# Optimization experiments

Hardware: AMD Instinct MI355X
Metric: run time of the kernel (lower is better)

The kernel has to match this reference:

```python
import jax, jax.numpy as jnp
import numpy as np

N_NODES = 50000
N_EDGES = 600000
N_GRAPHS = 64


def _linear_init(key, fan_in, fan_out):
    # torch nn.Linear default: U(-1/sqrt(fan_in), 1/sqrt(fan_in))
    s = 1.0 / np.sqrt(fan_in)
    kw, kb = jax.random.split(key)
    W = jax.random.uniform(kw, (fan_in, fan_out), jnp.float32, -s, s)
    b = jax.random.uniform(kb, (fan_out,), jnp.float32, -s, s)
    return W, b


def setup_inputs() -> dict:
    key = jax.random.key(0)
    ks = jax.random.split(key, 7)
    x = jax.random.normal(ks[0], (N_NODES, 128), jnp.float32)
    edge_index = jax.random.randint(ks[1], (2, N_EDGES), 0, N_NODES, dtype=jnp.int32).astype(jnp.int64)
    batch = jnp.sort(jax.random.randint(ks[2], (N_NODES,), 0, N_GRAPHS, dtype=jnp.int32)).astype(jnp.int64)
    W1, b1 = _linear_init(ks[3], 128, 256)
    W2, b2 = _linear_init(ks[4], 256, 256)
    W3, b3 = _linear_init(ks[5], 256, 128)
    W4, b4 = _linear_init(ks[6], 128, 10)
    return dict(x=x, edge_index=edge_index, batch=batch,
                W1=W1, b1=b1, W2=W2, b2=b2, W3=W3, b3=b3, W4=W4, b4=b4)


def _gcn_conv(h, src, dst, W, b, n_nodes):
    # PyG GCNConv: add self-loops (src/dst already include them),
    # symmetric normalization D^{-1/2} (A+I) D^{-1/2} h W + b.
    h = h @ W                                      # [N, Cout]
    deg = jax.ops.segment_sum(jnp.ones(src.shape[0], h.dtype), dst, num_segments=n_nodes)
    dinv = jnp.where(deg > 0, jax.lax.rsqrt(deg), 0.0)
    norm = dinv[src] * dinv[dst]                   # [E+N]
    msg = h[src] * norm[:, None]                   # gather + scale per edge
    agg = jax.ops.segment_sum(msg, dst, num_segments=n_nodes)  # scatter-add
    return agg + b


def reference(x, edge_index, batch, W1, b1, W2, b2, W3, b3, W4, b4):
    n = x.shape[0]
    loops = jnp.arange(n, dtype=edge_index.dtype)
    src = jnp.concatenate([edge_index[0], loops])
    dst = jnp.concatenate([edge_index[1], loops])
    # GCNBlock (activate_last=True since dense layers follow)
    h = jax.nn.relu(_gcn_conv(x, src, dst, W1, b1, n))
    h = jax.nn.relu(_gcn_conv(h, src, dst, W2, b2, n))
    # global_mean_pool over batch segments
    sums = jax.ops.segment_sum(h, batch, num_segments=N_GRAPHS)          # [G, 256]
    counts = jax.ops.segment_sum(jnp.ones((n,), h.dtype), batch, num_segments=N_GRAPHS)
    g = sums / jnp.maximum(counts, 1.0)[:, None]
    # DenseBlock [256 -> 128 -> 10], activate_last=False
    g = jax.nn.relu(g @ W3 + b3)
    return g @ W4 + b4
```

## Files before the change

kernel.cpp:

```cpp
#include <hip/hip_runtime.h>

typedef unsigned short u16;
typedef unsigned int u32;
typedef __attribute__((ext_vector_type(8))) short s16x8;
typedef __attribute__((ext_vector_type(4))) float f32x4;

#define NN 50000
#define NE 600000
#define NG 64

__device__ __forceinline__ u16 f2bf(float f) {
    u32 u = __float_as_uint(f);
    u32 r = (u + 0x7fffu + ((u >> 16) & 1u)) >> 16;
    return (u16)r;
}
__device__ __forceinline__ float bf2f(u16 h) {
    return __uint_as_float(((u32)h) << 16);
}
__device__ __forceinline__ void gll16(const void* g, void* l) {
    __builtin_amdgcn_global_load_lds((const __attribute__((address_space(1))) u32*)g,
                                     (__attribute__((address_space(3))) u32*)l, 16, 0, 0);
}

__global__ void k_hist(const int* __restrict__ dst, int* __restrict__ cnt, int ne) {
    int e = blockIdx.x * blockDim.x + threadIdx.x;
    if (e < ne) atomicAdd(&cnt[dst[e]], 1);
}

__global__ __launch_bounds__(256)
void k_scan1(const int* __restrict__ cnt, int* __restrict__ bsum, int n) {
    int i = blockIdx.x * 256 + threadIdx.x;
    int v = (i < n) ? cnt[i] : 0;
#pragma unroll
    for (int off = 32; off > 0; off >>= 1) v += __shfl_down(v, off, 64);
    __shared__ int ws[4];
    int lane = threadIdx.x & 63, w = threadIdx.x >> 6;
    if (lane == 0) ws[w] = v;
    __syncthreads();
    if (threadIdx.x == 0) bsum[blockIdx.x] = ws[0] + ws[1] + ws[2] + ws[3];
}

__global__ __launch_bounds__(256)
void k_scan2(int* __restrict__ bsum, int nb) {
    int t = threadIdx.x;
    int v = (t < nb) ? bsum[t] : 0;
    int lane = t & 63, w = t >> 6;
    int inc = v;
#pragma unroll
    for (int off = 1; off < 64; off <<= 1) {
        int x = __shfl_up(inc, off, 64);
        if (lane >= off) inc += x;
    }
    __shared__ int wtot[4];
    if (lane == 63) wtot[w] = inc;
    __syncthreads();
    int wo = 0;
    for (int j = 0; j < w; ++j) wo += wtot[j];
    if (t < nb) bsum[t] = wo + inc - v;
}

__global__ __launch_bounds__(256)
void k_scan3(const int* __restrict__ cnt, const int* __restrict__ boff,
             int* __restrict__ rowptr, int* __restrict__ cursor,
             float* __restrict__ dinv, int n) {
    int i = blockIdx.x * 256 + threadIdx.x;
    int v = (i < n) ? cnt[i] : 0;
    int lane = threadIdx.x & 63, w = threadIdx.x >> 6;
    int inc = v;
#pragma unroll
    for (int off = 1; off < 64; off <<= 1) {
        int x = __shfl_up(inc, off, 64);
        if (lane >= off) inc += x;
    }
    __shared__ int wtot[4];
    if (lane == 63) wtot[w] = inc;
    __syncthreads();
    int wo = boff[blockIdx.x];
    for (int j = 0; j < w; ++j) wo += wtot[j];
    if (i < n) {
        int excl = wo + inc - v;
        rowptr[i] = excl;
        cursor[i] = excl;
        dinv[i] = rsqrtf(1.0f + (float)v);
        if (i == n - 1) rowptr[n] = excl + v;
    }
}

__global__ void k_fill(const int* __restrict__ src, const int* __restrict__ dst,
                       int* __restrict__ cursor, int* __restrict__ csr_src, int ne) {
    int e = blockIdx.x * blockDim.x + threadIdx.x;
    if (e < ne) {
        int pos = atomicAdd(&cursor[dst[e]], 1);
        csr_src[pos] = src[e];
    }
}

__device__ __forceinline__ void wsplit_one(const float* W, u16* Whi, u16* Wlo, int K, int N, int idx) {
    int n = idx / K, k = idx - n * K;
    float w = W[(size_t)k * N + n];
    u16 hi = f2bf(w);
    u16 lo = f2bf(w - bf2f(hi));
    Whi[idx] = hi;
    Wlo[idx] = lo;
}

__global__ __launch_bounds__(256)
void k_preamble(const float* __restrict__ x, u16* __restrict__ xbf,
                const float* __restrict__ W1, u16* __restrict__ w1hi, u16* __restrict__ w1lo,
                const float* __restrict__ W2, u16* __restrict__ w2hi, u16* __restrict__ w2lo,
                float* __restrict__ sums, int* __restrict__ cnt,
                const int* __restrict__ batch, float* __restrict__ counts) {
    const int XB = (NN * 32 + 255) / 256;
    const int CB = (NN + 255) / 256;
    int b = blockIdx.x, t = threadIdx.x;
    if (b < XB) {
        int i = b * 256 + t;
        if (i < NN * 32) {
            float4 v = ((const float4*)x)[i];
            ushort4 o;
            o.x = f2bf(v.x); o.y = f2bf(v.y); o.z = f2bf(v.z); o.w = f2bf(v.w);
            ((ushort4*)xbf)[i] = o;
        }
        return;
    }
    b -= XB;
    if (b < 128) { wsplit_one(W1, w1hi, w1lo, 128, 256, b * 256 + t); return; }
    b -= 128;
    if (b < 256) { wsplit_one(W2, w2hi, w2lo, 256, 256, b * 256 + t); return; }
    b -= 256;
    if (b < 64) { sums[b * 256 + t] = 0.f; return; }
    b -= 64;
    if (b < CB) {
        int i = b * 256 + t;
        if (i < NN) cnt[i] = 0;
        return;
    }
    b -= CB;
    if (b == 0) {
        __shared__ int lb[65];
        if (t <= 64) {
            int lo = 0, hi = NN;
            while (lo < hi) {
                int mid = (lo + hi) >> 1;
                if (batch[mid] < t) lo = mid + 1; else hi = mid;
            }
            lb[t] = lo;
        }
        __syncthreads();
        if (t < 64) counts[t] = (float)(lb[t + 1] - lb[t]);
    }
}

template<int C>
__global__ __launch_bounds__(256)
void k_agg_gather(const int* __restrict__ rowptr, const int* __restrict__ csr_src,
                  const float* __restrict__ dinv, const u16* __restrict__ hb,
                  u16* __restrict__ out, int n) {
    constexpr int V = C / 64;
    int node = (blockIdx.x * blockDim.x + threadIdx.x) >> 6;
    int lane = threadIdx.x & 63;
    if (node >= n) return;
    int beg = rowptr[node], end = rowptr[node + 1];
    int m = end - beg;
    float di = dinv[node];
    float a0[V], a1[V];
    if constexpr (V == 4) {
        uint2 v = ((const uint2*)hb)[(size_t)node * 64 + lane];
        a0[0] = bf2f((u16)v.x) * di; a0[1] = bf2f((u16)(v.x >> 16)) * di;
        a0[2] = bf2f((u16)v.y) * di; a0[3] = bf2f((u16)(v.y >> 16)) * di;
        a1[0] = a1[1] = a1[2] = a1[3] = 0.f;
    } else {
        u32 v = ((const u32*)hb)[(size_t)node * 64 + lane];
        a0[0] = bf2f((u16)v) * di; a0[1] = bf2f((u16)(v >> 16)) * di;
        a1[0] = a1[1] = 0.f;
    }
    for (int base = 0; base < m; base += 64) {
        int c = m - base; if (c > 64) c = 64;
        int sid = 0; float w = 0.f;
        if (lane < c) { sid = csr_src[beg + base + lane]; w = dinv[sid]; }
        int e = 0;
        for (; e + 4 <= c; e += 4) {
            int   s0 = __shfl(sid, e, 64),   s1 = __shfl(sid, e + 1, 64);
            int   s2 = __shfl(sid, e + 2, 64), s3 = __shfl(sid, e + 3, 64);
            float w0 = __shfl(w, e, 64),     w1 = __shfl(w, e + 1, 64);
            float w2 = __shfl(w, e + 2, 64), w3 = __shfl(w, e + 3, 64);
            if constexpr (V == 4) {
                uint2 v0 = ((const uint2*)hb)[(size_t)s0 * 64 + lane];
                uint2 v1 = ((const uint2*)hb)[(size_t)s1 * 64 + lane];
                uint2 v2 = ((const uint2*)hb)[(size_t)s2 * 64 + lane];
                uint2 v3 = ((const uint2*)hb)[(size_t)s3 * 64 + lane];
                a0[0] += bf2f((u16)v0.x) * w0 + bf2f((u16)v2.x) * w2;
                a0[1] += bf2f((u16)(v0.x >> 16)) * w0 + bf2f((u16)(v2.x >> 16)) * w2;
                a0[2] += bf2f((u16)v0.y) * w0 + bf2f((u16)v2.y) * w2;
                a0[3] += bf2f((u16)(v0.y >> 16)) * w0 + bf2f((u16)(v2.y >> 16)) * w2;
                a1[0] += bf2f((u16)v1.x) * w1 + bf2f((u16)v3.x) * w3;
                a1[1] += bf2f((u16)(v1.x >> 16)) * w1 + bf2f((u16)(v3.x >> 16)) * w3;
                a1[2] += bf2f((u16)v1.y) * w1 + bf2f((u16)v3.y) * w3;
                a1[3] += bf2f((u16)(v1.y >> 16)) * w1 + bf2f((u16)(v3.y >> 16)) * w3;
            } else {
                u32 v0 = ((const u32*)hb)[(size_t)s0 * 64 + lane];
                u32 v1 = ((const u32*)hb)[(size_t)s1 * 64 + lane];
                u32 v2 = ((const u32*)hb)[(size_t)s2 * 64 + lane];
                u32 v3 = ((const u32*)hb)[(size_t)s3 * 64 + lane];
                a0[0] += bf2f((u16)v0) * w0 + bf2f((u16)v2) * w2;
                a0[1] += bf2f((u16)(v0 >> 16)) * w0 + bf2f((u16)(v2 >> 16)) * w2;
                a1[0] += bf2f((u16)v1) * w1 + bf2f((u16)v3) * w3;
                a1[1] += bf2f((u16)(v1 >> 16)) * w1 + bf2f((u16)(v3 >> 16)) * w3;
            }
        }
        for (; e < c; ++e) {
            int s0 = __shfl(sid, e, 64);
            float w0 = __shfl(w, e, 64);
            if constexpr (V == 4) {
                uint2 v0 = ((const uint2*)hb)[(size_t)s0 * 64 + lane];
                a0[0] += bf2f((u16)v0.x) * w0; a0[1] += bf2f((u16)(v0.x >> 16)) * w0;
                a0[2] += bf2f((u16)v0.y) * w0; a0[3] += bf2f((u16)(v0.y >> 16)) * w0;
            } else {
                u32 v0 = ((const u32*)hb)[(size_t)s0 * 64 + lane];
                a0[0] += bf2f((u16)v0) * w0; a0[1] += bf2f((u16)(v0 >> 16)) * w0;
            }
        }
    }
    if constexpr (V == 4) {
        uint2 o;
        o.x = (u32)f2bf((a0[0] + a1[0]) * di) | ((u32)f2bf((a0[1] + a1[1]) * di) << 16);
        o.y = (u32)f2bf((a0[2] + a1[2]) * di) | ((u32)f2bf((a0[3] + a1[3]) * di) << 16);
        ((uint2*)out)[(size_t)node * 64 + lane] = o;
    } else {
        ((u32*)out)[(size_t)node * 64 + lane] =
            (u32)f2bf((a0[0] + a1[0]) * di) | ((u32)f2bf((a0[1] + a1[1]) * di) << 16);
    }
}

__device__ __forceinline__ void stage_tile(u16* ldsbuf, const u16* A, const u16* Bhi,
                                           const u16* Blo, int bm, int k0, int M, int K,
                                           int wid, int lane) {
#pragma unroll
    for (int i = 0; i < 5; ++i) {
        int c = wid + 8 * i;
        const u16* gp;
        u32 lbase;
        if (c < 8) {
            int s = c * 64 + lane;
            int kga = s >> 7, row = s & 127;
            int rg = bm + row; if (rg >= M) rg = M - 1;
            gp = A + (size_t)rg * K + k0 + kga * 8;
            lbase = c * 512;
        } else if (c < 24) {
            int cc = c - 8;
            int s = cc * 64 + lane;
            int kgb = s >> 8, col = s & 255;
            gp = Bhi + (size_t)col * K + k0 + kgb * 8;
            lbase = 4096 + cc * 512;
        } else {
            int cc = c - 24;
            int s = cc * 64 + lane;
            int kgb = s >> 8, col = s & 255;
            gp = Blo + (size_t)col * K + k0 + kgb * 8;
            lbase = 12288 + cc * 512;
        }
        gll16(gp, ldsbuf + lbase);
    }
}

template<bool POOL>
__global__ __launch_bounds__(512)
void k_gemm_mfma(const u16* __restrict__ A, const u16* __restrict__ Bhi,
                 const u16* __restrict__ Blo,
                 const float* __restrict__ bias, u16* __restrict__ out_bf,
                 const int* __restrict__ batch, float* __restrict__ pool,
                 int M, int K) {
    __shared__ u16 lds[2][20480];
    const int tid = threadIdx.x, lane = tid & 63, wid = tid >> 6;
    const int bm = blockIdx.x * 128;
    const int wr = (wid >> 2) * 64, wc = (wid & 3) * 64;
    const int lr = lane & 15, kg = lane >> 4;

    f32x4 acc[4][4];
#pragma unroll
    for (int i = 0; i < 4; ++i)
#pragma unroll
        for (int j = 0; j < 4; ++j) acc[i][j] = (f32x4){0.f, 0.f, 0.f, 0.f};

    const int nt = K >> 5;
    stage_tile(lds[0], A, Bhi, Blo, bm, 0, M, K, wid, lane);
    __syncthreads();

    for (int t = 0; t < nt; ++t) {
        int cur = t & 1;
        if (t + 1 < nt)
            stage_tile(lds[cur ^ 1], A, Bhi, Blo, bm, (t + 1) << 5, M, K, wid, lane);
        const u16* lb = lds[cur];
        s16x8 a[4];
#pragma unroll
        for (int fm = 0; fm < 4; ++fm)
            a[fm] = *(const s16x8*)&lb[(u32)(kg * 128 + wr + fm * 16 + lr) * 8];
#pragma unroll
        for (int fn = 0; fn < 4; ++fn) {
            int col = wc + fn * 16 + lr;
            u32 sb = (u32)(kg * 256 + col) * 8;
            s16x8 bhi = *(const s16x8*)&lb[4096 + sb];
            s16x8 blo = *(const s16x8*)&lb[12288 + sb];
#pragma unroll
            for (int fm = 0; fm < 4; ++fm) {
                acc[fm][fn] = __builtin_amdgcn_mfma_f32_16x16x32_bf16(a[fm], bhi, acc[fm][fn], 0, 0, 0);
                acc[fm][fn] = __builtin_amdgcn_mfma_f32_16x16x32_bf16(a[fm], blo, acc[fm][fn], 0, 0, 0);
            }
        }
        __syncthreads();
    }

#pragma unroll
    for (int fn = 0; fn < 4; ++fn) {
        int col = wc + fn * 16 + lr;
        float bv = bias[col];
        if (!POOL) {
#pragma unroll
            for (int fm = 0; fm < 4; ++fm) {
                int rbase = bm + wr + fm * 16 + kg * 4;
#pragma unroll
                for (int r = 0; r < 4; ++r) {
                    int row = rbase + r;
                    if (row < M)
                        out_bf[(size_t)row * 256 + col] = f2bf(fmaxf(acc[fm][fn][r] + bv, 0.f));
                }
            }
        } else {
            int gcur = -1;
            float run = 0.f;
#pragma unroll
            for (int fm = 0; fm < 4; ++fm) {
                int rbase = bm + wr + fm * 16 + kg * 4;
#pragma unroll
                for (int r = 0; r < 4; ++r) {
                    int row = rbase + r;
                    if (row < M) {
                        int g = batch[row];
                        float v = fmaxf(acc[fm][fn][r] + bv, 0.f);
                        if (g != gcur) {
                            if (gcur >= 0) atomicAdd(&pool[gcur * 256 + col], run);
                            gcur = g;
                            run = 0.f;
                        }
                        run += v;
                    }
                }
            }
            if (gcur >= 0) atomicAdd(&pool[gcur * 256 + col], run);
        }
    }
}

__global__ __launch_bounds__(128)
void k_dense(const float* __restrict__ sums, const float* __restrict__ counts,
             const float* __restrict__ W3, const float* __restrict__ b3,
             const float* __restrict__ W4, const float* __restrict__ b4,
             float* __restrict__ out) {
    __shared__ float g[256];
    __shared__ float hid[128];
    int gi = blockIdx.x;
    int t = threadIdx.x;
    float inv = 1.0f / fmaxf(counts[gi], 1.0f);
    for (int c = t; c < 256; c += 128) g[c] = sums[gi * 256 + c] * inv;
    __syncthreads();
    float acc = b3[t];
    for (int k = 0; k < 256; ++k) acc += g[k] * W3[k * 128 + t];
    hid[t] = fmaxf(acc, 0.0f);
    __syncthreads();
    if (t < 10) {
        float o = b4[t];
        for (int k = 0; k < 128; ++k) o += hid[k] * W4[k * 10 + t];
        out[gi * 10 + t] = o;
    }
}

extern "C" void kernel_launch(void* const* d_in, const int* in_sizes, int n_in,
                              void* d_out, int out_size, void* d_ws, size_t ws_size,
                              hipStream_t stream) {
    const float* x   = (const float*)d_in[0];
    const int*  eidx = (const int*)d_in[1];
    const int*  batch= (const int*)d_in[2];
    const float* W1 = (const float*)d_in[3];
    const float* b1 = (const float*)d_in[4];
    const float* W2 = (const float*)d_in[5];
    const float* b2 = (const float*)d_in[6];
    const float* W3 = (const float*)d_in[7];
    const float* b3 = (const float*)d_in[8];
    const float* W4 = (const float*)d_in[9];
    const float* b4 = (const float*)d_in[10];
    float* out = (float*)d_out;

    const int N = NN, E = NE, G = NG;
    const int* src = eidx;
    const int* dst = eidx + E;
    const int NB = (N + 255) / 256;

    char* p = (char*)d_ws;
    auto alloc = [&](size_t bytes) { char* r = p; p += (bytes + 255) & ~(size_t)255; return r; };
    u16*   h1bf   = (u16*)alloc((size_t)N * 256 * 2);
    u16*   xbf    = (u16*)alloc((size_t)N * 128 * 2);
    float* dinv   = (float*)alloc((size_t)N * 4);
    float* sums   = (float*)alloc((size_t)G * 256 * 4);
    float* counts = (float*)alloc((size_t)G * 4);
    int*   cnt    = (int*)alloc((size_t)N * 4);
    int*   rowptr = (int*)alloc((size_t)(N + 1) * 4);
    int*   bsum   = (int*)alloc((size_t)NB * 4);
    int*   csr    = (int*)alloc((size_t)E * 4);
    u16*   agg1   = (u16*)alloc((size_t)N * 128 * 2);
    u16*   agg2   = (u16*)alloc((size_t)N * 256 * 2);
    u16*   w1hi   = (u16*)alloc((size_t)256 * 128 * 2);
    u16*   w1lo   = (u16*)alloc((size_t)256 * 128 * 2);
    u16*   w2hi   = (u16*)alloc((size_t)256 * 256 * 2);
    u16*   w2lo   = (u16*)alloc((size_t)256 * 256 * 2);
    int*   cursor = cnt;

    const int XB = (NN * 32 + 255) / 256;
    const int CB = (NN + 255) / 256;
    int pre_blocks = XB + 128 + 256 + 64 + CB + 1;
    k_preamble<<<pre_blocks, 256, 0, stream>>>(x, xbf, W1, w1hi, w1lo, W2, w2hi, w2lo,
                                               sums, cnt, batch, counts);

    k_hist<<<(E + 255) / 256, 256, 0, stream>>>(dst, cnt, E);
    k_scan1<<<NB, 256, 0, stream>>>(cnt, bsum, N);
    k_scan2<<<1, 256, 0, stream>>>(bsum, NB);
    k_scan3<<<NB, 256, 0, stream>>>(cnt, bsum, rowptr, cursor, dinv, N);
    k_fill<<<(E + 255) / 256, 256, 0, stream>>>(src, dst, cursor, csr, E);

    k_agg_gather<128><<<(N + 3) / 4, 256, 0, stream>>>(rowptr, csr, dinv, xbf, agg1, N);
    int gblocks = (N + 127) / 128;
    k_gemm_mfma<false><<<gblocks, 512, 0, stream>>>(agg1, w1hi, w1lo, b1, h1bf,
                                                    nullptr, nullptr, N, 128);

    k_agg_gather<256><<<(N + 3) / 4, 256, 0, stream>>>(rowptr, csr, dinv, h1bf, agg2, N);
    k_gemm_mfma<true><<<gblocks, 512, 0, stream>>>(agg2, w2hi, w2lo, b2, nullptr,
                                                   batch, sums, N, 256);

    k_dense<<<G, 128, 0, stream>>>(sums, counts, W3, b3, W4, b4, out);
}
```

Before: 241.9 us.

## Pre-tile weights for direct MFMA register loads and stage only A in LDS

Weight hi/lo splits are now written in a k-group-tiled layout (8 consecutive k per column), so GEMM waves can load B fragments straight from global/L2 into registers instead of staging them through LDS. LDS now holds only the A tile, using an XOR swizzle to avoid bank conflicts. Shared memory per block drops sharply and launch bounds request 4 blocks per CU to raise occupancy. The cost is repeated global reads of B by every block, which now rely on cache hits, and the B loads are not double-buffered.

```diff
diff --git a/kernel.cpp b/kernel.cpp
--- a/kernel.cpp
+++ b/kernel.cpp
@@ -95,13 +95,18 @@
     }
 }
 
-__device__ __forceinline__ void wsplit_one(const float* W, u16* Whi, u16* Wlo, int K, int N, int idx) {
-    int n = idx / K, k = idx - n * K;
-    float w = W[(size_t)k * N + n];
-    u16 hi = f2bf(w);
-    u16 lo = f2bf(w - bf2f(hi));
-    Whi[idx] = hi;
-    Wlo[idx] = lo;
+__device__ __forceinline__ void wsplit_tiled(const float* __restrict__ W,
+                                             u16* __restrict__ hi, u16* __restrict__ lo,
+                                             int gid) {
+    int n = gid & 255, kgrp = gid >> 8;
+    int kbase = kgrp * 8;
+#pragma unroll
+    for (int j = 0; j < 8; ++j) {
+        float w = W[(size_t)(kbase + j) * 256 + n];
+        u16 h = f2bf(w);
+        hi[(size_t)gid * 8 + j] = h;
+        lo[(size_t)gid * 8 + j] = f2bf(w - bf2f(h));
+    }
 }
 
 __global__ __launch_bounds__(256)
@@ -124,10 +129,10 @@
         return;
     }
     b -= XB;
-    if (b < 128) { wsplit_one(W1, w1hi, w1lo, 128, 256, b * 256 + t); return; }
-    b -= 128;
-    if (b < 256) { wsplit_one(W2, w2hi, w2lo, 256, 256, b * 256 + t); return; }
-    b -= 256;
+    if (b < 16) { wsplit_tiled(W1, w1hi, w1lo, b * 256 + t); return; }
+    b -= 16;
+    if (b < 32) { wsplit_tiled(W2, w2hi, w2lo, b * 256 + t); return; }
+    b -= 32;
     if (b < 64) { sums[b * 256 + t] = 0.f; return; }
     b -= 64;
     if (b < CB) {
@@ -232,50 +237,25 @@
     }
 }
 
-__device__ __forceinline__ void stage_tile(u16* ldsbuf, const u16* A, const u16* Bhi,
-                                           const u16* Blo, int bm, int k0, int M, int K,
-                                           int wid, int lane) {
-#pragma unroll
-    for (int i = 0; i < 5; ++i) {
-        int c = wid + 8 * i;
-        const u16* gp;
-        u32 lbase;
-        if (c < 8) {
-            int s = c * 64 + lane;
-            int kga = s >> 7, row = s & 127;
-            int rg = bm + row; if (rg >= M) rg = M - 1;
-            gp = A + (size_t)rg * K + k0 + kga * 8;
-            lbase = c * 512;
-        } else if (c < 24) {
-            int cc = c - 8;
-            int s = cc * 64 + lane;
-            int kgb = s >> 8, col = s & 255;
-            gp = Bhi + (size_t)col * K + k0 + kgb * 8;
-            lbase = 4096 + cc * 512;
-        } else {
-            int cc = c - 24;
-            int s = cc * 64 + lane;
-            int kgb = s >> 8, col = s & 255;
-            gp = Blo + (size_t)col * K + k0 + kgb * 8;
-            lbase = 12288 + cc * 512;
-        }
-        gll16(gp, ldsbuf + lbase);
-    }
-}
-
 template<bool POOL>
-__global__ __launch_bounds__(512)
+__global__ __launch_bounds__(512, 4)
 void k_gemm_mfma(const u16* __restrict__ A, const u16* __restrict__ Bhi,
                  const u16* __restrict__ Blo,
                  const float* __restrict__ bias, u16* __restrict__ out_bf,
                  const int* __restrict__ batch, float* __restrict__ pool,
                  int M, int K) {
-    __shared__ u16 lds[2][20480];
+    __shared__ u16 ldsA[2][4096];
     const int tid = threadIdx.x, lane = tid & 63, wid = tid >> 6;
     const int bm = blockIdx.x * 128;
     const int wr = (wid >> 2) * 64, wc = (wid & 3) * 64;
     const int lr = lane & 15, kg = lane >> 4;
 
+    const int srow = wid * 16 + (lane >> 2);
+    const int sslot = lane & 3;
+    const int ssw = (srow ^ (srow >> 2)) & 3;
+    int srg = bm + srow; if (srg >= M) srg = M - 1;
+    const u16* sbase = A + (size_t)srg * K + ((sslot ^ ssw) << 3);
+
     f32x4 acc[4][4];
 #pragma unroll
     for (int i = 0; i < 4; ++i)
@@ -283,30 +263,35 @@
         for (int j = 0; j < 4; ++j) acc[i][j] = (f32x4){0.f, 0.f, 0.f, 0.f};
 
     const int nt = K >> 5;
-    stage_tile(lds[0], A, Bhi, Blo, bm, 0, M, K, wid, lane);
+    gll16(sbase, &ldsA[0][wid * 512]);
     __syncthreads();
 
     for (int t = 0; t < nt; ++t) {
         int cur = t & 1;
         if (t + 1 < nt)
-            stage_tile(lds[cur ^ 1], A, Bhi, Blo, bm, (t + 1) << 5, M, K, wid, lane);
-        const u16* lb = lds[cur];
+            gll16(sbase + ((t + 1) << 5), &ldsA[cur ^ 1][wid * 512]);
+
+        s16x8 bh[4], bl[4];
+#pragma unroll
+        for (int fn = 0; fn < 4; ++fn) {
+            size_t off = ((size_t)((t << 2) + kg) * 256 + wc + fn * 16 + lr) * 8;
+            bh[fn] = *(const s16x8*)&Bhi[off];
+            bl[fn] = *(const s16x8*)&Blo[off];
+        }
+        const u16* lb = ldsA[cur];
         s16x8 a[4];
 #pragma unroll
-        for (int fm = 0; fm < 4; ++fm)
-            a[fm] = *(const s16x8*)&lb[(u32)(kg * 128 + wr + fm * 16 + lr) * 8];
-#pragma unroll
-        for (int fn = 0; fn < 4; ++fn) {
-            int col = wc + fn * 16 + lr;
-            u32 sb = (u32)(kg * 256 + col) * 8;
-            s16x8 bhi = *(const s16x8*)&lb[4096 + sb];
-            s16x8 blo = *(const s16x8*)&lb[12288 + sb];
+        for (int fm = 0; fm < 4; ++fm) {
+            int r = wr + fm * 16 + lr;
+            a[fm] = *(const s16x8*)&lb[r * 32 + ((kg ^ ((r ^ (r >> 2)) & 3)) << 3)];
+        }
+#pragma unroll
+        for (int fn = 0; fn < 4; ++fn)
 #pragma unroll
             for (int fm = 0; fm < 4; ++fm) {
-                acc[fm][fn] = __builtin_amdgcn_mfma_f32_16x16x32_bf16(a[fm], bhi, acc[fm][fn], 0, 0, 0);
-                acc[fm][fn] = __builtin_amdgcn_mfma_f32_16x16x32_bf16(a[fm], blo, acc[fm][fn], 0, 0, 0);
-            }
-        }
+                acc[fm][fn] = __builtin_amdgcn_mfma_f32_16x16x32_bf16(a[fm], bh[fn], acc[fm][fn], 0, 0, 0);
+                acc[fm][fn] = __builtin_amdgcn_mfma_f32_16x16x32_bf16(a[fm], bl[fn], acc[fm][fn], 0, 0, 0);
+            }
         __syncthreads();
     }
 
@@ -416,7 +401,7 @@
 
     const int XB = (NN * 32 + 255) / 256;
     const int CB = (NN + 255) / 256;
-    int pre_blocks = XB + 128 + 256 + 64 + CB + 1;
+    int pre_blocks = XB + 16 + 32 + 64 + CB + 1;
     k_preamble<<<pre_blocks, 256, 0, stream>>>(x, xbf, W1, w1hi, w1lo, W2, w2hi, w2lo,
                                                sums, cnt, batch, counts);
 
```

Result: faster. 224.0 us (-7.4%).
